# Optimization experiments

Hardware: AMD Instinct MI355X
Metric: run time of the kernel (lower is better)

The kernel has to match this reference:

```python
import jax, jax.numpy as jnp
import numpy as np

B, L, E = 4, 2048, 1024
H, DH = 16, 64          # num_heads, head_dim; hidden = H*DH = 1024
HID = H * DH
EPS = 1e-5


def setup_inputs() -> dict:
    key = jax.random.key(0)
    ks = jax.random.split(key, 16)
    s = 0.02
    return {
        "emb": jax.random.normal(ks[0], (B, L, E), jnp.float32),
        "Wa": jax.random.normal(ks[1], (H, E, DH), jnp.float32) * s,
        "ba": jax.random.normal(ks[2], (H, DH), jnp.float32) * s,
        "Wb": jax.random.normal(ks[3], (H, E, DH), jnp.float32) * s,
        "bb": jax.random.normal(ks[4], (H, DH), jnp.float32) * s,
        "WD": jax.random.normal(ks[5], (H, E, DH), jnp.float32) * s,
        "bD": jax.random.normal(ks[6], (H, DH), jnp.float32) * s,
        "WC": jax.random.normal(ks[7], (H, DH, DH), jnp.float32) * s,
        "bC": jax.random.normal(ks[8], (H, DH), jnp.float32) * s,
        "ffn1_w": jax.random.normal(ks[9], (HID, 4 * HID), jnp.float32) * s,
        "ffn1_b": jnp.zeros((4 * HID,), jnp.float32),
        "ffn2_w": jax.random.normal(ks[10], (4 * HID, HID), jnp.float32) * s,
        "ffn2_b": jnp.zeros((HID,), jnp.float32),
        "proj_w": jax.random.normal(ks[11], (HID, HID), jnp.float32) * s,
        "proj_b": jnp.zeros((HID,), jnp.float32),
        "ln_g": jnp.ones((HID,), jnp.float32),
        "ln_b": jnp.zeros((HID,), jnp.float32),
    }


def _layernorm(x, g, b):
    mu = jnp.mean(x, -1, keepdims=True)
    var = jnp.mean(jnp.square(x - mu), -1, keepdims=True)
    return (x - mu) * jax.lax.rsqrt(var + EPS) * g + b


def reference(emb, Wa, ba, Wb, bb, WD, bD, WC, bC,
              ffn1_w, ffn1_b, ffn2_w, ffn2_b, proj_w, proj_b, ln_g, ln_b):
    # per-head gates/inputs for all timesteps at once: [B, L, H, DH]
    a = jnp.tanh(jnp.einsum('ble,hed->blhd', emb, Wa) + ba)
    b = jnp.einsum('ble,hed->blhd', emb, Wb) + bb

    # affine recurrence h_t = a_t * h_{t-1} + b_t, h_0 = 0 -> parallel scan over L
    def comb(c1, c2):
        a1, b1 = c1
        a2, b2 = c2
        return a1 * a2, a2 * b1 + b2

    _, h = jax.lax.associative_scan(comb, (a, b), axis=1)  # [B, L, H, DH]

    d = jnp.einsum('ble,hed->blhd', emb, WD) + bD
    head_out = (jnp.einsum('blhd,hdf->blhf', h, WC) + bC) * d  # [B, L, H, DH]
    z = head_out.reshape(B, L, HID)

    u = z + _layernorm(z, ln_g, ln_b)
    ffn = jax.nn.gelu(u @ ffn1_w + ffn1_b, approximate=False) @ ffn2_w + ffn2_b
    return (u + ffn) @ proj_w + proj_b
```

## Files before the change

kernel.cpp:

```cpp
#include <hip/hip_runtime.h>
#include <hip/hip_bf16.h>
#include <math.h>

#define B_   4
#define L_   2048
#define E_   1024
#define H_   16
#define DH_  64
#define HID_ 1024
#define ROWS (B_*L_)
#define NCH  16
#define CLEN (L_/NCH)

typedef __attribute__((ext_vector_type(8))) short short8;
typedef __attribute__((ext_vector_type(4))) float f32x4;

__device__ __forceinline__ unsigned short f2bf(float f) {
  union { float f; unsigned int i; } v; v.f = f;
  unsigned int r = v.i + 0x7fffu + ((v.i >> 16) & 1u);
  return (unsigned short)(r >> 16);
}

__device__ __forceinline__ void gload16(const unsigned short* g, unsigned short* l) {
  __builtin_amdgcn_global_load_lds((const __attribute__((address_space(1))) void*)g,
                                   (__attribute__((address_space(3))) void*)l, 16, 0, 0);
}

__global__ void cast_f32_bf16(const float* __restrict__ src, unsigned short* __restrict__ dst, int n) {
  int i = (blockIdx.x * 256 + threadIdx.x) * 4;
  if (i < n) {
    float4 v = *(const float4*)(src + i);
    ushort4 o;
    o.x = f2bf(v.x); o.y = f2bf(v.y); o.z = f2bf(v.z); o.w = f2bf(v.w);
    *(ushort4*)(dst + i) = o;
  }
}

__global__ void transpose_cast(const float* __restrict__ src, unsigned short* __restrict__ dst,
                               int R, int C, int dstBase) {
  __shared__ float tile[32][33];
  src += (size_t)blockIdx.z * R * C;
  int dstRow0 = dstBase + blockIdx.z * C;
  int rb = blockIdx.x * 32, cb = blockIdx.y * 32;
  for (int i = threadIdx.y; i < 32; i += 8)
    tile[i][threadIdx.x] = src[(size_t)(rb + i) * C + cb + threadIdx.x];
  __syncthreads();
  for (int i = threadIdx.y; i < 32; i += 8)
    dst[(size_t)(dstRow0 + cb + i) * R + rb + threadIdx.x] = f2bf(tile[threadIdx.x][i]);
}

__global__ void build_bias(const float* __restrict__ ba, const float* __restrict__ bb,
                           const float* __restrict__ bD, float* __restrict__ bias) {
  int i = blockIdx.x * 256 + threadIdx.x;
  const float* src = (i < 1024) ? ba : ((i < 2048) ? bb : bD);
  bias[i] = src[i & 1023];
}

__global__ void build_wcblk(const float* __restrict__ WC, unsigned short* __restrict__ dst) {
  int i = blockIdx.x * 256 + threadIdx.x;
  int col = i >> 10, k = i & 1023;
  int hc = col >> 6, hk = k >> 6;
  float v = (hc == hk) ? WC[(size_t)hc * 4096 + (k & 63) * 64 + (col & 63)] : 0.f;
  dst[i] = f2bf(v);
}

#define EPI_GATES 0
#define EPI_GELU  1
#define EPI_RES   2
#define EPI_OUT   3
#define EPI_HEAD  4

template<int EPI>
__device__ __forceinline__ void epi_store(float xa, int rr, int cc, int N,
                                          const float* __restrict__ bias,
                                          const float* __restrict__ aux,
                                          void* __restrict__ out) {
  float x = xa + bias[cc];
  if (EPI == EPI_GATES) {
    if (cc < HID_) x = tanhf(x);
    ((float*)out)[(size_t)rr * N + cc] = x;
  } else if (EPI == EPI_GELU) {
    x = 0.5f * x * (1.f + erff(x * 0.70710678118654752f));
    ((unsigned short*)out)[(size_t)rr * N + cc] = f2bf(x);
  } else if (EPI == EPI_RES) {
    x += aux[(size_t)rr * N + cc];
    ((unsigned short*)out)[(size_t)rr * N + cc] = f2bf(x);
  } else if (EPI == EPI_HEAD) {
    x *= aux[(size_t)rr * 3072 + cc];
    ((float*)out)[(size_t)rr * N + cc] = x;
  } else {
    ((float*)out)[(size_t)rr * N + cc] = x;
  }
}

template<int EPI>
__global__ __launch_bounds__(256)
void gemm_bt(const unsigned short* __restrict__ A, const unsigned short* __restrict__ Bt,
             const float* __restrict__ bias, const float* __restrict__ aux,
             void* __restrict__ out, int M, int N, int K) {
  __shared__ unsigned short lA[128 * 32];
  __shared__ unsigned short lB[128 * 32];
  const int tid = threadIdx.x;
  const int w = tid >> 6, l = tid & 63;
  const int row0 = blockIdx.y * 128, col0 = blockIdx.x * 128;

  const int rA0 = w * 16 + (l >> 2);
  const int rA1 = (4 + w) * 16 + (l >> 2);
  const int koff = (l & 3) * 8;
  const unsigned short* gA0 = A + (size_t)(row0 + rA0) * K + koff;
  const unsigned short* gA1 = A + (size_t)(row0 + rA1) * K + koff;
  const unsigned short* gB0 = Bt + (size_t)(col0 + rA0) * K + koff;
  const unsigned short* gB1 = Bt + (size_t)(col0 + rA1) * K + koff;
  unsigned short* lA0 = lA + w * 512;
  unsigned short* lA1 = lA + (4 + w) * 512;
  unsigned short* lB0 = lB + w * 512;
  unsigned short* lB1 = lB + (4 + w) * 512;

  const int wr = (w >> 1) * 64, wc = (w & 1) * 64;
  f32x4 acc[4][4];
  #pragma unroll
  for (int m = 0; m < 4; m++)
    #pragma unroll
    for (int n = 0; n < 4; n++) acc[m][n] = (f32x4){0.f, 0.f, 0.f, 0.f};

  const int arow = wr + (l & 15);
  const int brow = wc + (l & 15);
  const int kg = (l >> 4) * 8;

  for (int kt = 0; kt < K; kt += 32) {
    __syncthreads();
    gload16(gA0 + kt, lA0);
    gload16(gA1 + kt, lA1);
    gload16(gB0 + kt, lB0);
    gload16(gB1 + kt, lB1);
    __syncthreads();
    short8 af[4], bfr[4];
    #pragma unroll
    for (int m = 0; m < 4; m++) af[m]  = *(const short8*)(lA + (arow + m * 16) * 32 + kg);
    #pragma unroll
    for (int n = 0; n < 4; n++) bfr[n] = *(const short8*)(lB + (brow + n * 16) * 32 + kg);
    #pragma unroll
    for (int m = 0; m < 4; m++)
      #pragma unroll
      for (int n = 0; n < 4; n++)
        acc[m][n] = __builtin_amdgcn_mfma_f32_16x16x32_bf16(af[m], bfr[n], acc[m][n], 0, 0, 0);
  }

  const int er = row0 + wr + ((l >> 4) << 2);
  const int ec = col0 + wc + (l & 15);
  #pragma unroll
  for (int m = 0; m < 4; m++)
    #pragma unroll
    for (int n = 0; n < 4; n++)
      #pragma unroll
      for (int j = 0; j < 4; j++)
        epi_store<EPI>(acc[m][n][j], er + m * 16 + j, ec + n * 16, N, bias, aux, out);
}

template<int EPI>
__global__ __launch_bounds__(512, 2)
void gemm256(const unsigned short* __restrict__ A, const unsigned short* __restrict__ Bt,
             const float* __restrict__ bias, const float* __restrict__ aux,
             void* __restrict__ out, int M, int N, int K) {
  __shared__ unsigned short lds[2][2][256 * 64];
  const int tid = threadIdx.x;
  const int w = tid >> 6, l = tid & 63;
  const int wm = w >> 2, wn = w & 3;
  const int row0 = blockIdx.y * 256, col0 = blockIdx.x * 256;
  const int lr = l & 15, kg = (l >> 4) << 3;
  const int wmb = wm * 128, wnb = wn * 64;
  const int T = K >> 6, nIter = T >> 1;

  const int srow = w * 8 + (l >> 3);
  const int kswz = (((l & 7) ^ (l >> 3)) << 3);

  f32x4 acc[8][4];
  #pragma unroll
  for (int m = 0; m < 8; m++)
    #pragma unroll
    for (int n = 0; n < 4; n++) acc[m][n] = (f32x4){0.f, 0.f, 0.f, 0.f};

  short8 a[4][2], b0[2][2], b1[2][2];

  auto stA = [&](int buf, int hh, int kt) {
    const unsigned short* g = A + (size_t)(row0 + hh * 128 + srow) * K + kt * 64 + kswz;
    unsigned short* d = &lds[buf][0][hh * 8192 + w * 512];
    gload16(g, d);
    gload16(g + (size_t)64 * K, d + 4096);
  };
  auto stB = [&](int buf, int hh, int kt) {
    const unsigned short* g = Bt + (size_t)(col0 + hh * 128 + srow) * K + kt * 64 + kswz;
    unsigned short* d = &lds[buf][1][hh * 8192 + w * 512];
    gload16(g, d);
    gload16(g + (size_t)64 * K, d + 4096);
  };

#define RD_A(LP, mh) { _Pragma("unroll") for (int mf = 0; mf < 4; ++mf) { _Pragma("unroll") for (int ks = 0; ks < 2; ++ks) { \
      int r = wmb + (mh) * 64 + mf * 16 + lr; int k = ks * 32 + kg; \
      a[mf][ks] = *(const short8*)((LP) + r * 64 + (k ^ ((r & 7) << 3))); } } }
#define RD_B(dst, LP, nh) { _Pragma("unroll") for (int nf = 0; nf < 2; ++nf) { _Pragma("unroll") for (int ks = 0; ks < 2; ++ks) { \
      int r = wnb + (nh) * 32 + nf * 16 + lr; int k = ks * 32 + kg; \
      dst[nf][ks] = *(const short8*)((LP) + r * 64 + (k ^ ((r & 7) << 3))); } } }
#define MMA(bb, MB, NB) \
    __builtin_amdgcn_s_setprio(1); \
    _Pragma("unroll") for (int mf = 0; mf < 4; ++mf) { _Pragma("unroll") for (int nf = 0; nf < 2; ++nf) { _Pragma("unroll") for (int ks = 0; ks < 2; ++ks) { \
      acc[(MB) + mf][(NB) + nf] = __builtin_amdgcn_mfma_f32_16x16x32_bf16(a[mf][ks], bb[nf][ks], acc[(MB) + mf][(NB) + nf], 0, 0, 0); } } } \
    __builtin_amdgcn_s_setprio(0);

  stA(0, 0, 0); stA(0, 1, 0); stB(0, 0, 0); stB(0, 1, 0);
  stB(1, 0, 1); stA(1, 0, 1);
  asm volatile("s_waitcnt vmcnt(4)" ::: "memory");
  __builtin_amdgcn_s_barrier();

  for (int i = 0; i < nIter; ++i) {
    const int t0 = 2 * i, t1 = t0 + 1;
    const bool pf = (i + 1 < nIter);
    const unsigned short* LA0 = lds[0][0];
    const unsigned short* LB0 = lds[0][1];
    const unsigned short* LA1 = lds[1][0];
    const unsigned short* LB1 = lds[1][1];

    RD_A(LA0, 0); RD_B(b0, LB0, 0);
    stA(1, 1, t1); stB(1, 1, t1);
    __builtin_amdgcn_s_barrier();
    MMA(b0, 0, 0);
    __builtin_amdgcn_s_barrier();
    RD_B(b1, LB0, 1);
    __builtin_amdgcn_s_barrier();
    MMA(b1, 0, 2);
    __builtin_amdgcn_s_barrier();
    RD_A(LA0, 1);
    if (pf) stB(0, 0, t0 + 2);
    __builtin_amdgcn_s_barrier();
    MMA(b0, 4, 0);
    __builtin_amdgcn_s_barrier();
    if (pf) stA(0, 0, t0 + 2);
    if (pf) asm volatile("s_waitcnt vmcnt(4)" ::: "memory");
    else    asm volatile("s_waitcnt vmcnt(0)" ::: "memory");
    __builtin_amdgcn_s_barrier();
    MMA(b1, 4, 2);
    __builtin_amdgcn_s_barrier();

    RD_A(LA1, 0); RD_B(b0, LB1, 0);
    if (pf) { stA(0, 1, t0 + 2); stB(0, 1, t0 + 2); }
    __builtin_amdgcn_s_barrier();
    MMA(b0, 0, 0);
    __builtin_amdgcn_s_barrier();
    RD_B(b1, LB1, 1);
    __builtin_amdgcn_s_barrier();
    MMA(b1, 0, 2);
    __builtin_amdgcn_s_barrier();
    RD_A(LA1, 1);
    if (pf) stB(1, 0, t1 + 2);
    __builtin_amdgcn_s_barrier();
    MMA(b0, 4, 0);
    __builtin_amdgcn_s_barrier();
    if (pf) stA(1, 0, t1 + 2);
    if (pf) asm volatile("s_waitcnt vmcnt(4)" ::: "memory");
    else    asm volatile("s_waitcnt vmcnt(0)" ::: "memory");
    __builtin_amdgcn_s_barrier();
    MMA(b1, 4, 2);
    __builtin_amdgcn_s_barrier();
  }
#undef RD_A
#undef RD_B
#undef MMA

  const int er = row0 + wmb + ((l >> 4) << 2);
  const int ec = col0 + wnb + lr;
  #pragma unroll
  for (int mi = 0; mi < 8; ++mi)
    #pragma unroll
    for (int ni = 0; ni < 4; ++ni)
      #pragma unroll
      for (int j = 0; j < 4; ++j)
        epi_store<EPI>(acc[mi][ni][j], er + mi * 16 + j, ec + ni * 16, N, bias, aux, out);
}

__global__ void scan_p1(const float* __restrict__ abd, float* __restrict__ aggA, float* __restrict__ aggB) {
  int id = blockIdx.x * 256 + threadIdx.x;
  int c = id & 1023;
  int chunk = (id >> 10) & (NCH - 1);
  int bb = id >> 14;
  const float* base = abd + (size_t)(bb * L_ + chunk * CLEN) * 3072;
  float Aa = 1.f, Bv = 0.f;
  #pragma unroll 4
  for (int t = 0; t < CLEN; ++t) {
    float a = base[(size_t)t * 3072 + c];
    float b = base[(size_t)t * 3072 + 1024 + c];
    Aa *= a;
    Bv = a * Bv + b;
  }
  int o = (chunk * B_ + bb) * 1024 + c;
  aggA[o] = Aa; aggB[o] = Bv;
}

__global__ void scan_p2(const float* __restrict__ aggA, const float* __restrict__ aggB,
                        float* __restrict__ hinit) {
  int id = blockIdx.x * 256 + threadIdx.x;
  float hc = 0.f;
  for (int ch = 0; ch < NCH; ++ch) {
    int o = ch * 4096 + id;
    hinit[o] = hc;
    hc = aggA[o] * hc + aggB[o];
  }
}

__global__ void scan_p3(const float* __restrict__ abd, const float* __restrict__ hinit,
                        unsigned short* __restrict__ hb16) {
  int id = blockIdx.x * 256 + threadIdx.x;
  int c = id & 1023;
  int chunk = (id >> 10) & (NCH - 1);
  int bb = id >> 14;
  const float* base = abd + (size_t)(bb * L_ + chunk * CLEN) * 3072;
  unsigned short* hb = hb16 + (size_t)(bb * L_ + chunk * CLEN) * 1024;
  float h = hinit[chunk * 4096 + bb * 1024 + c];
  #pragma unroll 4
  for (int t = 0; t < CLEN; ++t) {
    float a = base[(size_t)t * 3072 + c];
    float b = base[(size_t)t * 3072 + 1024 + c];
    h = a * h + b;
    hb[(size_t)t * 1024 + c] = f2bf(h);
  }
}

__global__ __launch_bounds__(256)
void ln_res(const float* __restrict__ z, const float* __restrict__ lg, const float* __restrict__ lb,
            float* __restrict__ u32, unsigned short* __restrict__ u16) {
  int row = blockIdx.x;
  int t = threadIdx.x;
  const float4 zv = *(const float4*)(z + (size_t)row * 1024 + t * 4);
  float s = zv.x + zv.y + zv.z + zv.w;
  float sq = zv.x * zv.x + zv.y * zv.y + zv.z * zv.z + zv.w * zv.w;
  #pragma unroll
  for (int o = 32; o > 0; o >>= 1) { s += __shfl_down(s, o); sq += __shfl_down(sq, o); }
  __shared__ float ps[4], pq[4];
  if ((t & 63) == 0) { ps[t >> 6] = s; pq[t >> 6] = sq; }
  __syncthreads();
  s = ps[0] + ps[1] + ps[2] + ps[3];
  sq = pq[0] + pq[1] + pq[2] + pq[3];
  float mu = s * (1.f / 1024.f);
  float var = sq * (1.f / 1024.f) - mu * mu;
  float rs = rsqrtf(var + 1e-5f);
  const float4 gv = *(const float4*)(lg + t * 4);
  const float4 bv = *(const float4*)(lb + t * 4);
  float4 o;
  o.x = zv.x + (zv.x - mu) * rs * gv.x + bv.x;
  o.y = zv.y + (zv.y - mu) * rs * gv.y + bv.y;
  o.z = zv.z + (zv.z - mu) * rs * gv.z + bv.z;
  o.w = zv.w + (zv.w - mu) * rs * gv.w + bv.w;
  *(float4*)(u32 + (size_t)row * 1024 + t * 4) = o;
  ushort4 ob; ob.x = f2bf(o.x); ob.y = f2bf(o.y); ob.z = f2bf(o.z); ob.w = f2bf(o.w);
  *(ushort4*)(u16 + (size_t)row * 1024 + t * 4) = ob;
}

extern "C" void kernel_launch(void* const* d_in, const int* in_sizes, int n_in,
                              void* d_out, int out_size, void* d_ws, size_t ws_size,
                              hipStream_t stream) {
  const float* emb    = (const float*)d_in[0];
  const float* Wa     = (const float*)d_in[1];
  const float* ba     = (const float*)d_in[2];
  const float* Wb     = (const float*)d_in[3];
  const float* bb     = (const float*)d_in[4];
  const float* WD     = (const float*)d_in[5];
  const float* bD     = (const float*)d_in[6];
  const float* WC     = (const float*)d_in[7];
  const float* bC     = (const float*)d_in[8];
  const float* ffn1_w = (const float*)d_in[9];
  const float* ffn1_b = (const float*)d_in[10];
  const float* ffn2_w = (const float*)d_in[11];
  const float* ffn2_b = (const float*)d_in[12];
  const float* proj_w = (const float*)d_in[13];
  const float* proj_b = (const float*)d_in[14];
  const float* ln_g   = (const float*)d_in[15];
  const float* ln_b   = (const float*)d_in[16];

  char* p = (char*)d_ws;
  auto alloc = [&](size_t bytes) { char* r = p; p += (bytes + 255) & ~(size_t)255; return (void*)r; };

  float* abd   = (float*)alloc((size_t)ROWS * 3072 * 4);
  unsigned short* hb16 = (unsigned short*)alloc((size_t)ROWS * 1024 * 2);
  float* zbuf  = (float*)alloc((size_t)ROWS * 1024 * 4);
  float* u32   = (float*)alloc((size_t)ROWS * 1024 * 4);
  unsigned short* u16  = (unsigned short*)alloc((size_t)ROWS * 1024 * 2);
  unsigned short* embb = (unsigned short*)alloc((size_t)ROWS * 1024 * 2);
  unsigned short* wcat = (unsigned short*)alloc((size_t)3072 * 1024 * 2);
  unsigned short* f1t  = (unsigned short*)alloc((size_t)4096 * 1024 * 2);
  unsigned short* f2t  = (unsigned short*)alloc((size_t)4096 * 1024 * 2);
  unsigned short* pjt  = (unsigned short*)alloc((size_t)1024 * 1024 * 2);
  unsigned short* wcblk= (unsigned short*)alloc((size_t)1024 * 1024 * 2);
  float* biascat = (float*)alloc(3072 * 4);
  float* aggA  = (float*)alloc(65536 * 4);
  float* aggB  = (float*)alloc(65536 * 4);
  float* hinit = (float*)alloc(65536 * 4);
  unsigned short* gbuf = (unsigned short*)abd;
  unsigned short* vbuf = (unsigned short*)zbuf;

  dim3 tb(32, 8);
  cast_f32_bf16<<<ROWS * 1024 / 1024, 256, 0, stream>>>(emb, embb, ROWS * 1024);
  build_bias<<<12, 256, 0, stream>>>(ba, bb, bD, biascat);
  build_wcblk<<<1024 * 1024 / 256, 256, 0, stream>>>(WC, wcblk);
  transpose_cast<<<dim3(E_ / 32, DH_ / 32, H_), tb, 0, stream>>>(Wa, wcat, E_, DH_, 0);
  transpose_cast<<<dim3(E_ / 32, DH_ / 32, H_), tb, 0, stream>>>(Wb, wcat, E_, DH_, 1024);
  transpose_cast<<<dim3(E_ / 32, DH_ / 32, H_), tb, 0, stream>>>(WD, wcat, E_, DH_, 2048);
  transpose_cast<<<dim3(1024 / 32, 4096 / 32, 1), tb, 0, stream>>>(ffn1_w, f1t, 1024, 4096, 0);
  transpose_cast<<<dim3(4096 / 32, 1024 / 32, 1), tb, 0, stream>>>(ffn2_w, f2t, 4096, 1024, 0);
  transpose_cast<<<dim3(1024 / 32, 1024 / 32, 1), tb, 0, stream>>>(proj_w, pjt, 1024, 1024, 0);

  gemm256<EPI_GATES><<<dim3(3072 / 256, ROWS / 256), 512, 0, stream>>>(
      embb, wcat, biascat, nullptr, abd, ROWS, 3072, 1024);

  scan_p1<<<65536 / 256, 256, 0, stream>>>(abd, aggA, aggB);
  scan_p2<<<4096 / 256, 256, 0, stream>>>(aggA, aggB, hinit);
  scan_p3<<<65536 / 256, 256, 0, stream>>>(abd, hinit, hb16);

  gemm_bt<EPI_HEAD><<<dim3(1024 / 128, ROWS / 128), 256, 0, stream>>>(
      hb16, wcblk, bC, abd + 2048, zbuf, ROWS, 1024, 1024);

  ln_res<<<ROWS, 256, 0, stream>>>(zbuf, ln_g, ln_b, u32, u16);

  gemm256<EPI_GELU><<<dim3(4096 / 256, ROWS / 256), 512, 0, stream>>>(
      u16, f1t, ffn1_b, nullptr, gbuf, ROWS, 4096, 1024);
  gemm_bt<EPI_RES><<<dim3(1024 / 128, ROWS / 128), 256, 0, stream>>>(
      gbuf, f2t, ffn2_b, u32, vbuf, ROWS, 1024, 4096);
  gemm_bt<EPI_OUT><<<dim3(1024 / 128, ROWS / 128), 256, 0, stream>>>(
      vbuf, pjt, proj_b, nullptr, (float*)d_out, ROWS, 1024, 1024);
}
```

Before: 605.2 us.

## Exploit block-diagonal head GEMM, store gates in bf16, add 256x128 GEMM and tile swizzle

The head-output GEMM now reads only the 128-wide K slice covering each output tile's diagonal heads, instead of multiplying by a mostly-zero 1024x1024 block-diagonal matrix. Gate outputs are stored as interleaved bf16 (a,b) pairs plus a separate bf16 d buffer, which cuts scan and epilogue memory traffic at some precision cost. The FFN2 and projection GEMMs move to a new 256x128 double-buffered 512-thread kernel. All GEMMs also remap workgroup IDs with a stride-8 swizzle for better cache locality.

```diff
diff --git a/kernel.cpp b/kernel.cpp
--- a/kernel.cpp
+++ b/kernel.cpp
@@ -19,6 +19,9 @@
   union { float f; unsigned int i; } v; v.f = f;
   unsigned int r = v.i + 0x7fffu + ((v.i >> 16) & 1u);
   return (unsigned short)(r >> 16);
+}
+__device__ __forceinline__ float bf2f(unsigned int u) {
+  union { unsigned int i; float f; } v; v.i = u << 16; return v.f;
 }
 
 __device__ __forceinline__ void gload16(const unsigned short* g, unsigned short* l) {
@@ -56,11 +59,10 @@
   bias[i] = src[i & 1023];
 }
 
-__global__ void build_wcblk(const float* __restrict__ WC, unsigned short* __restrict__ dst) {
+__global__ void build_wcd(const float* __restrict__ WC, unsigned short* __restrict__ dst) {
   int i = blockIdx.x * 256 + threadIdx.x;
-  int col = i >> 10, k = i & 1023;
-  int hc = col >> 6, hk = k >> 6;
-  float v = (hc == hk) ? WC[(size_t)hc * 4096 + (k & 63) * 64 + (col & 63)] : 0.f;
+  int c = i >> 7, kl = i & 127;
+  float v = ((kl >> 6) == ((c >> 6) & 1)) ? WC[(size_t)(c >> 6) * 4096 + (kl & 63) * 64 + (c & 63)] : 0.f;
   dst[i] = f2bf(v);
 }
 
@@ -73,44 +75,55 @@
 template<int EPI>
 __device__ __forceinline__ void epi_store(float xa, int rr, int cc, int N,
                                           const float* __restrict__ bias,
-                                          const float* __restrict__ aux,
-                                          void* __restrict__ out) {
+                                          const void* __restrict__ aux,
+                                          void* __restrict__ out, void* __restrict__ out2) {
   float x = xa + bias[cc];
   if (EPI == EPI_GATES) {
-    if (cc < HID_) x = tanhf(x);
-    ((float*)out)[(size_t)rr * N + cc] = x;
+    if (cc < HID_) {
+      x = tanhf(x);
+      ((unsigned short*)out)[(size_t)rr * 2048 + (cc << 1)] = f2bf(x);
+    } else if (cc < 2048) {
+      ((unsigned short*)out)[(size_t)rr * 2048 + ((cc - 1024) << 1) + 1] = f2bf(x);
+    } else {
+      ((unsigned short*)out2)[(size_t)rr * 1024 + (cc - 2048)] = f2bf(x);
+    }
   } else if (EPI == EPI_GELU) {
     x = 0.5f * x * (1.f + erff(x * 0.70710678118654752f));
     ((unsigned short*)out)[(size_t)rr * N + cc] = f2bf(x);
   } else if (EPI == EPI_RES) {
-    x += aux[(size_t)rr * N + cc];
+    x += ((const float*)aux)[(size_t)rr * N + cc];
     ((unsigned short*)out)[(size_t)rr * N + cc] = f2bf(x);
   } else if (EPI == EPI_HEAD) {
-    x *= aux[(size_t)rr * 3072 + cc];
+    x *= bf2f(((const unsigned short*)aux)[(size_t)rr * 1024 + cc]);
     ((float*)out)[(size_t)rr * N + cc] = x;
   } else {
     ((float*)out)[(size_t)rr * N + cc] = x;
   }
 }
 
-template<int EPI>
+template<int EPI, int DIAG>
 __global__ __launch_bounds__(256)
-void gemm_bt(const unsigned short* __restrict__ A, const unsigned short* __restrict__ Bt,
-             const float* __restrict__ bias, const float* __restrict__ aux,
-             void* __restrict__ out, int M, int N, int K) {
+void gemm_bt(const unsigned short* __restrict__ A, int lda,
+             const unsigned short* __restrict__ Bt, int ldb,
+             const float* __restrict__ bias, const void* __restrict__ aux,
+             void* __restrict__ out, void* __restrict__ out2, int M, int N, int K) {
   __shared__ unsigned short lA[128 * 32];
   __shared__ unsigned short lB[128 * 32];
   const int tid = threadIdx.x;
   const int w = tid >> 6, l = tid & 63;
-  const int row0 = blockIdx.y * 128, col0 = blockIdx.x * 128;
+  const int gx = gridDim.x, nwg = gx * gridDim.y;
+  const int o = blockIdx.y * gx + blockIdx.x;
+  const int lin = (o & 7) * (nwg >> 3) + (o >> 3);
+  const int row0 = (lin / gx) * 128, col0 = (lin % gx) * 128;
+  const int kOff = DIAG ? col0 : 0;
 
   const int rA0 = w * 16 + (l >> 2);
   const int rA1 = (4 + w) * 16 + (l >> 2);
   const int koff = (l & 3) * 8;
-  const unsigned short* gA0 = A + (size_t)(row0 + rA0) * K + koff;
-  const unsigned short* gA1 = A + (size_t)(row0 + rA1) * K + koff;
-  const unsigned short* gB0 = Bt + (size_t)(col0 + rA0) * K + koff;
-  const unsigned short* gB1 = Bt + (size_t)(col0 + rA1) * K + koff;
+  const unsigned short* gA0 = A + (size_t)(row0 + rA0) * lda + kOff + koff;
+  const unsigned short* gA1 = A + (size_t)(row0 + rA1) * lda + kOff + koff;
+  const unsigned short* gB0 = Bt + (size_t)(col0 + rA0) * ldb + koff;
+  const unsigned short* gB1 = Bt + (size_t)(col0 + rA1) * ldb + koff;
   unsigned short* lA0 = lA + w * 512;
   unsigned short* lA1 = lA + (4 + w) * 512;
   unsigned short* lB0 = lB + w * 512;
@@ -154,22 +167,25 @@
     for (int n = 0; n < 4; n++)
       #pragma unroll
       for (int j = 0; j < 4; j++)
-        epi_store<EPI>(acc[m][n][j], er + m * 16 + j, ec + n * 16, N, bias, aux, out);
+        epi_store<EPI>(acc[m][n][j], er + m * 16 + j, ec + n * 16, N, bias, aux, out, out2);
 }
 
 template<int EPI>
 __global__ __launch_bounds__(512, 2)
 void gemm256(const unsigned short* __restrict__ A, const unsigned short* __restrict__ Bt,
-             const float* __restrict__ bias, const float* __restrict__ aux,
-             void* __restrict__ out, int M, int N, int K) {
+             const float* __restrict__ bias, const void* __restrict__ aux,
+             void* __restrict__ out, void* __restrict__ out2, int M, int N, int K) {
   __shared__ unsigned short lds[2][2][256 * 64];
   const int tid = threadIdx.x;
   const int w = tid >> 6, l = tid & 63;
   const int wm = w >> 2, wn = w & 3;
-  const int row0 = blockIdx.y * 256, col0 = blockIdx.x * 256;
+  const int gx = gridDim.x, nwg = gx * gridDim.y;
+  const int o = blockIdx.y * gx + blockIdx.x;
+  const int lin = (o & 7) * (nwg >> 3) + (o >> 3);
+  const int row0 = (lin / gx) * 256, col0 = (lin % gx) * 256;
   const int lr = l & 15, kg = (l >> 4) << 3;
   const int wmb = wm * 128, wnb = wn * 64;
-  const int T = K >> 6, nIter = T >> 1;
+  const int nIter = K >> 7;
 
   const int srow = w * 8 + (l >> 3);
   const int kswz = (((l & 7) ^ (l >> 3)) << 3);
@@ -274,20 +290,138 @@
     for (int ni = 0; ni < 4; ++ni)
       #pragma unroll
       for (int j = 0; j < 4; ++j)
-        epi_store<EPI>(acc[mi][ni][j], er + mi * 16 + j, ec + ni * 16, N, bias, aux, out);
-}
-
-__global__ void scan_p1(const float* __restrict__ abd, float* __restrict__ aggA, float* __restrict__ aggB) {
+        epi_store<EPI>(acc[mi][ni][j], er + mi * 16 + j, ec + ni * 16, N, bias, aux, out, out2);
+}
+
+template<int EPI>
+__global__ __launch_bounds__(512, 2)
+void gemm256x128(const unsigned short* __restrict__ A, const unsigned short* __restrict__ Bt,
+                 const float* __restrict__ bias, const void* __restrict__ aux,
+                 void* __restrict__ out, void* __restrict__ out2, int M, int N, int K) {
+  __shared__ unsigned short lA2[2][256 * 64];
+  __shared__ unsigned short lB2[2][128 * 64];
+  const int tid = threadIdx.x;
+  const int w = tid >> 6, l = tid & 63;
+  const int wm = w >> 1, wn = w & 1;
+  const int gx = gridDim.x, nwg = gx * gridDim.y;
+  const int o = blockIdx.y * gx + blockIdx.x;
+  const int lin = (o & 7) * (nwg >> 3) + (o >> 3);
+  const int row0 = (lin / gx) * 256, col0 = (lin % gx) * 128;
+  const int lr = l & 15, kg = (l >> 4) << 3;
+  const int nIter = K >> 7;
+
+  const int srow = w * 8 + (l >> 3);
+  const int kswz = (((l & 7) ^ (l >> 3)) << 3);
+
+  f32x4 acc[4][4];
+  #pragma unroll
+  for (int m = 0; m < 4; m++)
+    #pragma unroll
+    for (int n = 0; n < 4; n++) acc[m][n] = (f32x4){0.f, 0.f, 0.f, 0.f};
+
+  short8 a[2][2], b0[2][2], b1[2][2];
+
+  auto stA = [&](int buf, int hh, int kt) {
+    const unsigned short* g = A + (size_t)(row0 + hh * 128 + srow) * K + kt * 64 + kswz;
+    unsigned short* d = &lA2[buf][hh * 8192 + w * 512];
+    gload16(g, d);
+    gload16(g + (size_t)64 * K, d + 4096);
+  };
+  auto stB = [&](int buf, int hh, int kt) {
+    const unsigned short* g = Bt + (size_t)(col0 + hh * 64 + srow) * K + kt * 64 + kswz;
+    gload16(g, &lB2[buf][hh * 4096 + w * 512]);
+  };
+
+#define RDA2(buf, mh) { _Pragma("unroll") for (int mf = 0; mf < 2; ++mf) { _Pragma("unroll") for (int ks = 0; ks < 2; ++ks) { \
+      int r = wm * 64 + (mh) * 32 + mf * 16 + lr; int k = ks * 32 + kg; \
+      a[mf][ks] = *(const short8*)(&lA2[buf][r * 64 + (k ^ ((r & 7) << 3))]); } } }
+#define RDB2(dst, buf, nh) { _Pragma("unroll") for (int nf = 0; nf < 2; ++nf) { _Pragma("unroll") for (int ks = 0; ks < 2; ++ks) { \
+      int r = wn * 64 + (nh) * 32 + nf * 16 + lr; int k = ks * 32 + kg; \
+      dst[nf][ks] = *(const short8*)(&lB2[buf][r * 64 + (k ^ ((r & 7) << 3))]); } } }
+#define MMA2(bb, MB, NB) \
+    __builtin_amdgcn_s_setprio(1); \
+    _Pragma("unroll") for (int mf = 0; mf < 2; ++mf) { _Pragma("unroll") for (int nf = 0; nf < 2; ++nf) { _Pragma("unroll") for (int ks = 0; ks < 2; ++ks) { \
+      acc[(MB) + mf][(NB) + nf] = __builtin_amdgcn_mfma_f32_16x16x32_bf16(a[mf][ks], bb[nf][ks], acc[(MB) + mf][(NB) + nf], 0, 0, 0); } } } \
+    __builtin_amdgcn_s_setprio(0);
+
+  stA(0, 0, 0); stA(0, 1, 0); stB(0, 0, 0); stB(0, 1, 0);
+  stB(1, 0, 1); stA(1, 0, 1);
+  asm volatile("s_waitcnt vmcnt(3)" ::: "memory");
+  __builtin_amdgcn_s_barrier();
+
+  for (int i = 0; i < nIter; ++i) {
+    const int t0 = 2 * i, t1 = t0 + 1;
+    const bool pf = (i + 1 < nIter);
+
+    RDA2(0, 0); RDB2(b0, 0, 0);
+    stA(1, 1, t1); stB(1, 1, t1);
+    __builtin_amdgcn_s_barrier();
+    MMA2(b0, 0, 0);
+    __builtin_amdgcn_s_barrier();
+    RDB2(b1, 0, 1);
+    __builtin_amdgcn_s_barrier();
+    MMA2(b1, 0, 2);
+    __builtin_amdgcn_s_barrier();
+    RDA2(0, 1);
+    if (pf) stB(0, 0, t0 + 2);
+    __builtin_amdgcn_s_barrier();
+    MMA2(b0, 2, 0);
+    __builtin_amdgcn_s_barrier();
+    if (pf) stA(0, 0, t0 + 2);
+    if (pf) asm volatile("s_waitcnt vmcnt(3)" ::: "memory");
+    else    asm volatile("s_waitcnt vmcnt(0)" ::: "memory");
+    __builtin_amdgcn_s_barrier();
+    MMA2(b1, 2, 2);
+    __builtin_amdgcn_s_barrier();
+
+    RDA2(1, 0); RDB2(b0, 1, 0);
+    if (pf) { stA(0, 1, t0 + 2); stB(0, 1, t0 + 2); }
+    __builtin_amdgcn_s_barrier();
+    MMA2(b0, 0, 0);
+    __builtin_amdgcn_s_barrier();
+    RDB2(b1, 1, 1);
+    __builtin_amdgcn_s_barrier();
+    MMA2(b1, 0, 2);
+    __builtin_amdgcn_s_barrier();
+    RDA2(1, 1);
+    if (pf) stB(1, 0, t1 + 2);
+    __builtin_amdgcn_s_barrier();
+    MMA2(b0, 2, 0);
+    __builtin_amdgcn_s_barrier();
+    if (pf) stA(1, 0, t1 + 2);
+    if (pf) asm volatile("s_waitcnt vmcnt(3)" ::: "memory");
+    else    asm volatile("s_waitcnt vmcnt(0)" ::: "memory");
+    __builtin_amdgcn_s_barrier();
+    MMA2(b1, 2, 2);
+    __builtin_amdgcn_s_barrier();
+  }
+#undef RDA2
+#undef RDB2
+#undef MMA2
+
+  const int er = row0 + wm * 64 + ((l >> 4) << 2);
+  const int ec = col0 + wn * 64 + lr;
+  #pragma unroll
+  for (int mi = 0; mi < 4; ++mi)
+    #pragma unroll
+    for (int ni = 0; ni < 4; ++ni)
+      #pragma unroll
+      for (int j = 0; j < 4; ++j)
+        epi_store<EPI>(acc[mi][ni][j], er + mi * 16 + j, ec + ni * 16, N, bias, aux, out, out2);
+}
+
+__global__ void scan_p1(const unsigned short* __restrict__ ab16, float* __restrict__ aggA, float* __restrict__ aggB) {
   int id = blockIdx.x * 256 + threadIdx.x;
   int c = id & 1023;
   int chunk = (id >> 10) & (NCH - 1);
   int bb = id >> 14;
-  const float* base = abd + (size_t)(bb * L_ + chunk * CLEN) * 3072;
+  const unsigned short* base = ab16 + (size_t)(bb * L_ + chunk * CLEN) * 2048 + 2 * c;
   float Aa = 1.f, Bv = 0.f;
   #pragma unroll 4
   for (int t = 0; t < CLEN; ++t) {
-    float a = base[(size_t)t * 3072 + c];
-    float b = base[(size_t)t * 3072 + 1024 + c];
+    unsigned int v = *(const unsigned int*)(base + (size_t)t * 2048);
+    float a = bf2f(v & 0xffffu);
+    float b = bf2f(v >> 16);
     Aa *= a;
     Bv = a * Bv + b;
   }
@@ -306,19 +440,20 @@
   }
 }
 
-__global__ void scan_p3(const float* __restrict__ abd, const float* __restrict__ hinit,
+__global__ void scan_p3(const unsigned short* __restrict__ ab16, const float* __restrict__ hinit,
                         unsigned short* __restrict__ hb16) {
   int id = blockIdx.x * 256 + threadIdx.x;
   int c = id & 1023;
   int chunk = (id >> 10) & (NCH - 1);
   int bb = id >> 14;
-  const float* base = abd + (size_t)(bb * L_ + chunk * CLEN) * 3072;
+  const unsigned short* base = ab16 + (size_t)(bb * L_ + chunk * CLEN) * 2048 + 2 * c;
   unsigned short* hb = hb16 + (size_t)(bb * L_ + chunk * CLEN) * 1024;
   float h = hinit[chunk * 4096 + bb * 1024 + c];
   #pragma unroll 4
   for (int t = 0; t < CLEN; ++t) {
-    float a = base[(size_t)t * 3072 + c];
-    float b = base[(size_t)t * 3072 + 1024 + c];
+    unsigned int v = *(const unsigned int*)(base + (size_t)t * 2048);
+    float a = bf2f(v & 0xffffu);
+    float b = bf2f(v >> 16);
     h = a * h + b;
     hb[(size_t)t * 1024 + c] = f2bf(h);
   }
@@ -378,7 +513,8 @@
   char* p = (char*)d_ws;
   auto alloc = [&](size_t bytes) { char* r = p; p += (bytes + 255) & ~(size_t)255; return (void*)r; };
 
-  float* abd   = (float*)alloc((size_t)ROWS * 3072 * 4);
+  unsigned short* ab16 = (unsigned short*)alloc((size_t)ROWS * 2048 * 2);
+  unsigned short* d16  = (unsigned short*)alloc((size_t)ROWS * 1024 * 2);
   unsigned short* hb16 = (unsigned short*)alloc((size_t)ROWS * 1024 * 2);
   float* zbuf  = (float*)alloc((size_t)ROWS * 1024 * 4);
   float* u32   = (float*)alloc((size_t)ROWS * 1024 * 4);
@@ -388,18 +524,18 @@
   unsigned short* f1t  = (unsigned short*)alloc((size_t)4096 * 1024 * 2);
   unsigned short* f2t  = (unsigned short*)alloc((size_t)4096 * 1024 * 2);
   unsigned short* pjt  = (unsigned short*)alloc((size_t)1024 * 1024 * 2);
-  unsigned short* wcblk= (unsigned short*)alloc((size_t)1024 * 1024 * 2);
+  unsigned short* wcd  = (unsigned short*)alloc((size_t)1024 * 128 * 2);
   float* biascat = (float*)alloc(3072 * 4);
   float* aggA  = (float*)alloc(65536 * 4);
   float* aggB  = (float*)alloc(65536 * 4);
   float* hinit = (float*)alloc(65536 * 4);
-  unsigned short* gbuf = (unsigned short*)abd;
+  unsigned short* gbuf = ab16;
   unsigned short* vbuf = (unsigned short*)zbuf;
 
   dim3 tb(32, 8);
   cast_f32_bf16<<<ROWS * 1024 / 1024, 256, 0, stream>>>(emb, embb, ROWS * 1024);
   build_bias<<<12, 256, 0, stream>>>(ba, bb, bD, biascat);
-  build_wcblk<<<1024 * 1024 / 256, 256, 0, stream>>>(WC, wcblk);
+  build_wcd<<<1024 * 128 / 256, 256, 0, stream>>>(WC, wcd);
   transpose_cast<<<dim3(E_ / 32, DH_ / 32, H_), tb, 0, stream>>>(Wa, wcat, E_, DH_, 0);
   transpose_cast<<<dim3(E_ / 32, DH_ / 32, H_), tb, 0, stream>>>(Wb, wcat, E_, DH_, 1024);
   transpose_cast<<<dim3(E_ / 32, DH_ / 32, H_), tb, 0, stream>>>(WD, wcat, E_, DH_, 2048);
@@ -408,21 +544,21 @@
   transpose_cast<<<dim3(1024 / 32, 1024 / 32, 1), tb, 0, stream>>>(proj_w, pjt, 1024, 1024, 0);
 
   gemm256<EPI_GATES><<<dim3(3072 / 256, ROWS / 256), 512, 0, stream>>>(
-      embb, wcat, biascat, nullptr, abd, ROWS, 3072, 1024);
-
-  scan_p1<<<65536 / 256, 256, 0, stream>>>(abd, aggA, aggB);
+      embb, wcat, biascat, nullptr, ab16, d16, ROWS, 3072, 1024);
+
+  scan_p1<<<65536 / 256, 256, 0, stream>>>(ab16, aggA, aggB);
   scan_p2<<<4096 / 256, 256, 0, stream>>>(aggA, aggB, hinit);
-  scan_p3<<<65536 / 256, 256, 0, stream>>>(abd, hinit, hb16);
-
-  gemm_bt<EPI_HEAD><<<dim3(1024 / 128, ROWS / 128), 256, 0, stream>>>(
-      hb16, wcblk, bC, abd + 2048, zbuf, ROWS, 1024, 1024);
+  scan_p3<<<65536 / 256, 256, 0, stream>>>(ab16, hinit, hb16);
+
+  gemm_bt<EPI_HEAD, 1><<<dim3(1024 / 128, ROWS / 128), 256, 0, stream>>>(
+      hb16, 1024, wcd, 128, bC, d16, zbuf, nullptr, ROWS, 1024, 128);
 
   ln_res<<<ROWS, 256, 0, stream>>>(zbuf, ln_g, ln_b, u32, u16);
 
   gemm256<EPI_GELU><<<dim3(4096 / 256, ROWS / 256), 512, 0, stream>>>(
-      u16, f1t, ffn1_b, nullptr, gbuf, ROWS, 4096, 1024);
-  gemm_bt<EPI_RES><<<dim3(1024 / 128, ROWS / 128), 256, 0, stream>>>(
-      gbuf, f2t, ffn2_b, u32, vbuf, ROWS, 1024, 4096);
-  gemm_bt<EPI_OUT><<<dim3(1024 / 128, ROWS / 128), 256, 0, stream>>>(
-      vbuf, pjt, proj_b, nullptr, (float*)d_out, ROWS, 1024, 1024);
-}
+      u16, f1t, ffn1_b, nullptr, gbuf, nullptr, ROWS, 4096, 1024);
+  gemm256x128<EPI_RES><<<dim3(1024 / 128, ROWS / 256), 512, 0, stream>>>(
+      gbuf, f2t, ffn2_b, u32, vbuf, nullptr, ROWS, 1024, 4096);
+  gemm256x128<EPI_OUT><<<dim3(1024 / 128, ROWS / 256), 512, 0, stream>>>(
+      vbuf, pjt, proj_b, nullptr, (float*)d_out, nullptr, ROWS, 1024, 1024);
+}
```

Measured after the change: 553.9 us. 1.09x faster.
